# Performance work log

Measured on AMD Instinct MI355X. Metric: run time of the kernel, lower is better.

The kernel has to match this reference:

```python
import jax, jax.numpy as jnp
import numpy as np

D_MODEL = 1024
D_HIDDEN = 2048
BATCH = 2
SEQ = 4096


def setup_inputs() -> dict:
    key = jax.random.key(0)
    ks = jax.random.split(key, 14)
    d, h = D_MODEL, D_HIDDEN
    s_d = 1.0 / np.sqrt(d)
    s_h = 1.0 / np.sqrt(h)
    x = jax.random.normal(ks[0], (BATCH, SEQ, d), jnp.float32)
    W1 = jax.random.normal(ks[1], (d, d), jnp.float32) * s_d
    W2 = jax.random.normal(ks[2], (d, d), jnp.float32) * s_d
    Wlast = jax.random.normal(ks[3], (d, d), jnp.float32) * s_d
    conv_w = jax.random.normal(ks[4], (d, 1, 3), jnp.float32) * 0.5  # depthwise (O, I/g=1, K)
    conv_b = jnp.zeros((d,), jnp.float32)
    A = jax.random.normal(ks[5], (h,), jnp.float32)
    Wb = jax.random.normal(ks[6], (h, d), jnp.float32) * s_d
    bb = jnp.zeros((h,), jnp.float32)
    Wc = jax.random.normal(ks[7], (d, h), jnp.float32) * s_h
    bc = jnp.zeros((d,), jnp.float32)
    Wd = jax.random.normal(ks[8], (d, d), jnp.float32) * s_d
    bd = jnp.zeros((d,), jnp.float32)
    # small delta so cumsum(delta*A) over SEQ steps stays O(1) (avoids exp overflow)
    Wdelta = jax.random.normal(ks[9], (h, d), jnp.float32) * 0.01
    bdelta = jnp.full((h,), -8.0, jnp.float32)
    return dict(x=x, W1=W1, conv_w=conv_w, conv_b=conv_b, A=A, Wb=Wb, bb=bb,
                Wc=Wc, bc=bc, Wd=Wd, bd=bd, Wdelta=Wdelta, bdelta=bdelta,
                W2=W2, Wlast=Wlast)


def reference(x, W1, conv_w, conv_b, A, Wb, bb, Wc, bc, Wd, bd, Wdelta, bdelta, W2, Wlast):
    # x: [B, L, d]
    x1 = x @ W1.T  # linear1 (no bias)
    # depthwise conv1d, kernel 3, pad 1, groups = d_model
    xc = jax.lax.conv_general_dilated(
        x1.transpose(0, 2, 1), conv_w,
        window_strides=(1,), padding=[(1, 1)],
        feature_group_count=D_MODEL,
        dimension_numbers=('NCH', 'OIH', 'NCH')) + conv_b[None, :, None]
    xa = jax.nn.silu(xc.transpose(0, 2, 1))  # [B, L, d]
    # SSM: delta/A/B discretization + cumprod-cumsum scan along sequence
    delta = jax.nn.softplus(xa @ Wdelta.T + bdelta)  # [B, L, h]
    A_bar = jnp.exp(delta * A)
    B_bar = delta * (xa @ Wb.T + bb)
    A_cum = jnp.cumprod(A_bar, axis=1)
    h_st = jnp.cumsum(B_bar / A_cum, axis=1) * A_cum  # [B, L, h]
    out_ssm = (h_st @ Wc.T + bc) + (xa @ Wd.T + bd)  # [B, L, d]
    # gated residual
    x_res = jax.nn.silu(out_ssm @ W2.T)
    z = out_ssm * x_res
    return out_ssm + z @ Wlast.T
```

## Files before the change

kernel.cpp:

```cpp
#include <hip/hip_runtime.h>
#include <cstdint>
#include <cstddef>

#define DMODEL 1024
#define DH 2048
#define BATCH 2
#define SEQ 4096
#define MROWS (BATCH*SEQ)
#define CHUNK 64
#define NCHUNK (SEQ/CHUNK)

typedef unsigned short u16;
typedef unsigned int u32;
typedef __attribute__((ext_vector_type(8))) short bf16x8;
typedef __attribute__((ext_vector_type(4))) float f32x4;

__device__ __forceinline__ u16 f2bf(float f) {
    union { float f; unsigned u; } v; v.f = f;
    unsigned r = v.u + 0x7FFFu + ((v.u >> 16) & 1u);
    return (u16)(r >> 16);
}
__device__ __forceinline__ float bf2f(u16 h) {
    union { unsigned u; float f; } v; v.u = ((unsigned)h) << 16; return v.f;
}

__device__ __forceinline__ float softplus_fast(float x) {
    if (x < -4.f) return __expf(x);
    return (x > 0.f) ? (x + log1pf(__expf(-x))) : log1pf(__expf(x));
}
__device__ __forceinline__ float silu_fast(float v) {
    return v * __fdividef(1.f, 1.f + __expf(-v));
}

__global__ void cvt_bf16(const float* __restrict__ src, u16* __restrict__ dst, int n4) {
    int i = blockIdx.x * blockDim.x + threadIdx.x;
    if (i >= n4) return;
    const float4 v = reinterpret_cast<const float4*>(src)[i];
    ushort4 o;
    o.x = f2bf(v.x); o.y = f2bf(v.y); o.z = f2bf(v.z); o.w = f2bf(v.w);
    reinterpret_cast<ushort4*>(dst)[i] = o;
}

struct CvtArgs {
    const float* src[7];
    u16* dst[7];
    unsigned cum[8];
};
__global__ void cvt_multi(CvtArgs a) {
    const unsigned i = blockIdx.x * blockDim.x + threadIdx.x;
    if (i >= a.cum[7]) return;
    int s = 0;
    while (i >= a.cum[s+1]) ++s;
    const unsigned off = i - a.cum[s];
    const float4 v = reinterpret_cast<const float4*>(a.src[s])[off];
    ushort4 o;
    o.x = f2bf(v.x); o.y = f2bf(v.y); o.z = f2bf(v.z); o.w = f2bf(v.w);
    reinterpret_cast<ushort4*>(a.dst[s])[off] = o;
}

__device__ __forceinline__ void gload_lds16(const void* g, void* l) {
    __builtin_amdgcn_global_load_lds(
        (const __attribute__((address_space(1))) void*)g,
        (__attribute__((address_space(3))) void*)l,
        16, 0, 0);
}

template<int EP, bool TWOK, int BN>
__global__ __launch_bounds__(256, 4) void gemm_bt(
    const u16* __restrict__ A1, const u16* __restrict__ B1, int K1,
    const u16* __restrict__ A2, const u16* __restrict__ B2, int K2,
    float* __restrict__ C, u16* __restrict__ Cb, u16* __restrict__ Cb2,
    const float* __restrict__ bias, const float* __restrict__ bias2,
    const u16* __restrict__ aux,
    int M, int N)
{
    constexpr int FN   = BN / 32;
    constexpr int EPS  = BN + 4;
    constexpr int SMEM = (BN == 128) ? 40960 : 24576;
    __shared__ __align__(16) char smem[SMEM];
    u16* As = (u16*)smem;
    u16* Bs = (u16*)(smem + 16384);
    float* ep = (float*)smem;

    const int tid = threadIdx.x;

    const int nwg = gridDim.x * gridDim.y;
    int wg = blockIdx.y * gridDim.x + blockIdx.x;
    wg = (wg & 7) * (nwg >> 3) + (wg >> 3);
    const int stile = wg >> 6;
    const int t64   = wg & 63;
    const int nSn   = gridDim.x >> 3;
    const int sm = (nSn > 0) ? stile / nSn : stile;
    const int sn = (nSn > 0) ? stile - sm * nSn : 0;
    const int m0 = (sm * 8 + (t64 >> 3)) * 128;
    const int n0 = (sn * 8 + (t64 & 7)) * BN;

    const int wave = tid >> 6, lane = tid & 63;
    const int wr = (wave >> 1) * 64;
    const int wc = (wave & 1) * (BN / 2);
    const int fr = lane & 15, fq = lane >> 4;

    f32x4 acc[4][FN];
    #pragma unroll
    for (int m = 0; m < 4; m++)
        #pragma unroll
        for (int n = 0; n < FN; n++) acc[m][n] = f32x4{0.f, 0.f, 0.f, 0.f};

    auto run_seg = [&](const u16* __restrict__ A, const u16* __restrict__ B, int K) {
        const int nt = K >> 6;
        for (int t = 0; t < nt; ++t) {
            const int k0 = t << 6;
            #pragma unroll
            for (int i = 0; i < 4; ++i) {
                const int g = i*256 + tid;
                const int r = g >> 3;
                const int ch = (g & 7) ^ (r & 7);
                gload_lds16(A + (size_t)(m0 + r)*K + (k0 + ch*8), (char*)As + (size_t)g*16);
            }
            #pragma unroll
            for (int i = 0; i < BN/32; ++i) {
                const int g = i*256 + tid;
                const int r = g >> 3;
                const int ch = (g & 7) ^ (r & 7);
                gload_lds16(B + (size_t)(n0 + r)*K + (k0 + ch*8), (char*)Bs + (size_t)g*16);
            }
            __syncthreads();

            #pragma unroll
            for (int kk = 0; kk < 2; ++kk) {
                bf16x8 af[4], bfr[FN];
                #pragma unroll
                for (int m = 0; m < 4; m++) {
                    const int r = wr + m*16 + fr;
                    af[m] = *reinterpret_cast<const bf16x8*>(
                        (const char*)As + r*128 + (((kk*4 + fq) ^ (r & 7)) * 16));
                }
                #pragma unroll
                for (int n = 0; n < FN; n++) {
                    const int r = wc + n*16 + fr;
                    bfr[n] = *reinterpret_cast<const bf16x8*>(
                        (const char*)Bs + r*128 + (((kk*4 + fq) ^ (r & 7)) * 16));
                }
                #pragma unroll
                for (int m = 0; m < 4; m++)
                    #pragma unroll
                    for (int n = 0; n < FN; n++)
                        acc[m][n] = __builtin_amdgcn_mfma_f32_16x16x32_bf16(af[m], bfr[n], acc[m][n], 0, 0, 0);
            }
            __syncthreads();
        }
    };
    run_seg(A1, B1, K1);
    if constexpr (TWOK) run_seg(A2, B2, K2);

    const bool isDelta = (EP == 4) ? (n0 < DH) : false;
    #pragma unroll
    for (int c = 0; c < 2; ++c) {
        if ((wave >> 1) == c) {
            #pragma unroll
            for (int m = 0; m < 4; m++)
                #pragma unroll
                for (int n = 0; n < FN; n++) {
                    const int col = wc + n*16 + fr;
                    #pragma unroll
                    for (int j = 0; j < 4; j++)
                        ep[(m*16 + fq*4 + j)*EPS + col] = acc[m][n][j];
                }
        }
        __syncthreads();
        #pragma unroll
        for (int p = 0; p < BN/16; ++p) {
            const int idx = p*256 + tid;
            const int row = idx / (BN/4), c4 = idx % (BN/4);
            float4 v = *reinterpret_cast<const float4*>(&ep[row*EPS + c4*4]);
            const int rg   = m0 + c*64 + row;
            const int colg = n0 + c4*4;
            if constexpr (EP == 4) {
                const int cc = isDelta ? colg : (colg - DH);
                const float4 bv = *reinterpret_cast<const float4*>(
                    (isDelta ? bias : bias2) + cc);
                ushort4 o;
                if (isDelta) {
                    o.x = f2bf(softplus_fast(v.x + bv.x));
                    o.y = f2bf(softplus_fast(v.y + bv.y));
                    o.z = f2bf(softplus_fast(v.z + bv.z));
                    o.w = f2bf(softplus_fast(v.w + bv.w));
                } else {
                    o.x = f2bf(v.x + bv.x); o.y = f2bf(v.y + bv.y);
                    o.z = f2bf(v.z + bv.z); o.w = f2bf(v.w + bv.w);
                }
                *reinterpret_cast<ushort4*>((isDelta ? Cb : Cb2) + (size_t)rg*DH + cc) = o;
            } else {
                if (bias) {
                    const float4 b1 = *reinterpret_cast<const float4*>(bias + colg);
                    v.x += b1.x; v.y += b1.y; v.z += b1.z; v.w += b1.w;
                }
                if (bias2) {
                    const float4 b2 = *reinterpret_cast<const float4*>(bias2 + colg);
                    v.x += b2.x; v.y += b2.y; v.z += b2.z; v.w += b2.w;
                }
                const size_t gidx = (size_t)rg * N + colg;
                if constexpr (EP == 0) {
                    ushort4 o = { f2bf(v.x), f2bf(v.y), f2bf(v.z), f2bf(v.w) };
                    *reinterpret_cast<ushort4*>(Cb + gidx) = o;
                } else if constexpr (EP == 2) {
                    const ushort4 ab = *reinterpret_cast<const ushort4*>(aux + gidx);
                    ushort4 o = { f2bf(bf2f(ab.x) * silu_fast(v.x)),
                                  f2bf(bf2f(ab.y) * silu_fast(v.y)),
                                  f2bf(bf2f(ab.z) * silu_fast(v.z)),
                                  f2bf(bf2f(ab.w) * silu_fast(v.w)) };
                    *reinterpret_cast<ushort4*>(Cb + gidx) = o;
                } else {
                    const ushort4 ab = *reinterpret_cast<const ushort4*>(aux + gidx);
                    float4 o = { bf2f(ab.x) + v.x, bf2f(ab.y) + v.y,
                                 bf2f(ab.z) + v.z, bf2f(ab.w) + v.w };
                    *reinterpret_cast<float4*>(C + gidx) = o;
                }
            }
        }
        __syncthreads();
    }
}

__global__ void conv_silu8(const u16* __restrict__ x1, const float* __restrict__ cw,
                           const float* __restrict__ cb, u16* __restrict__ xab) {
    int t = blockIdx.x * blockDim.x + threadIdx.x;
    int c8  = t & (DMODEL/8 - 1);
    int row = t >> 7;
    int l = row & (SEQ - 1);
    const int c0 = c8 * 8;
    const size_t i0 = (size_t)row * DMODEL + c0;
    bf16x8 v0 = *reinterpret_cast<const bf16x8*>(x1 + i0);
    bf16x8 vm = {}; if (l > 0)       vm = *reinterpret_cast<const bf16x8*>(x1 + i0 - DMODEL);
    bf16x8 vp = {}; if (l < SEQ - 1) vp = *reinterpret_cast<const bf16x8*>(x1 + i0 + DMODEL);
    if (l == 0)       vm = bf16x8{};
    if (l == SEQ - 1) vp = bf16x8{};
    bf16x8 o;
    #pragma unroll
    for (int j = 0; j < 8; ++j) {
        const int c = c0 + j;
        float v = cw[c*3+0]*bf2f((u16)vm[j]) + cw[c*3+1]*bf2f((u16)v0[j])
                + cw[c*3+2]*bf2f((u16)vp[j]) + cb[c];
        o[j] = (short)f2bf(silu_fast(v));
    }
    *reinterpret_cast<bf16x8*>(xab + i0) = o;
}

__global__ void scan_chunks(const u16* __restrict__ delta, const u16* __restrict__ pBv,
                            const float* __restrict__ Avec,
                            float* __restrict__ cA, float* __restrict__ cB) {
    const int c = (blockIdx.x * blockDim.x + threadIdx.x) * 2;
    const int q = blockIdx.y;
    const int b = blockIdx.z;
    const float A0 = Avec[c], A1 = Avec[c+1];
    float hA0 = 1.f, hB0 = 0.f, hA1 = 1.f, hB1 = 0.f;
    size_t base = ((size_t)b*SEQ + q*CHUNK)*DH + c;
    for (int j = 0; j < CHUNK; ++j) {
        const u32 du = *reinterpret_cast<const u32*>(delta + base);
        const u32 pu = *reinterpret_cast<const u32*>(pBv + base);
        const float d0 = bf2f((u16)(du & 0xFFFF)), d1 = bf2f((u16)(du >> 16));
        const float p0 = bf2f((u16)(pu & 0xFFFF)), p1 = bf2f((u16)(pu >> 16));
        const float a0 = __expf(d0 * A0), a1 = __expf(d1 * A1);
        hA0 *= a0; hB0 = a0*hB0 + d0*p0;
        hA1 *= a1; hB1 = a1*hB1 + d1*p1;
        base += DH;
    }
    size_t o = ((size_t)b*NCHUNK + q)*DH + c;
    cA[o] = hA0; cA[o+1] = hA1;
    cB[o] = hB0; cB[o+1] = hB1;
}

__global__ void scan_prefix(const float* __restrict__ cA, const float* __restrict__ cB,
                            float* __restrict__ cH) {
    const int t = blockIdx.x * blockDim.x + threadIdx.x;
    const int b = t >> 11;
    const int c = t & (DH - 1);
    float h = 0.f;
    size_t o = ((size_t)b*NCHUNK)*DH + c;
    float a = cA[o], bb = cB[o];
    for (int q = 0; q < NCHUNK; ++q) {
        const size_t on = o + DH;
        float a2 = 0.f, b2 = 0.f;
        if (q + 1 < NCHUNK) { a2 = cA[on]; b2 = cB[on]; }
        cH[o] = h;
        h = a*h + bb;
        a = a2; bb = b2; o = on;
    }
}

__global__ void scan_apply(const u16* __restrict__ delta, const u16* __restrict__ pBv,
                           const float* __restrict__ Avec, const float* __restrict__ cH,
                           u16* __restrict__ hstb) {
    const int c = (blockIdx.x * blockDim.x + threadIdx.x) * 2;
    const int q = blockIdx.y;
    const int b = blockIdx.z;
    const float A0 = Avec[c], A1 = Avec[c+1];
    const size_t oh = ((size_t)b*NCHUNK + q)*DH + c;
    float h0 = cH[oh], h1 = cH[oh+1];
    size_t base = ((size_t)b*SEQ + q*CHUNK)*DH + c;
    for (int j = 0; j < CHUNK; ++j) {
        const u32 du = *reinterpret_cast<const u32*>(delta + base);
        const u32 pu = *reinterpret_cast<const u32*>(pBv + base);
        const float d0 = bf2f((u16)(du & 0xFFFF)), d1 = bf2f((u16)(du >> 16));
        const float p0 = bf2f((u16)(pu & 0xFFFF)), p1 = bf2f((u16)(pu >> 16));
        const float a0 = __expf(d0 * A0), a1 = __expf(d1 * A1);
        h0 = a0*h0 + d0*p0;
        h1 = a1*h1 + d1*p1;
        const u32 hv = (u32)f2bf(h0) | ((u32)f2bf(h1) << 16);
        *reinterpret_cast<u32*>(hstb + base) = hv;
        base += DH;
    }
}

extern "C" void kernel_launch(void* const* d_in, const int* in_sizes, int n_in,
                              void* d_out, int out_size, void* d_ws, size_t ws_size,
                              hipStream_t stream) {
    const float* x      = (const float*)d_in[0];
    const float* W1     = (const float*)d_in[1];
    const float* conv_w = (const float*)d_in[2];
    const float* conv_b = (const float*)d_in[3];
    const float* Avec   = (const float*)d_in[4];
    const float* Wb     = (const float*)d_in[5];
    const float* bb     = (const float*)d_in[6];
    const float* Wc     = (const float*)d_in[7];
    const float* bc     = (const float*)d_in[8];
    const float* Wd     = (const float*)d_in[9];
    const float* bd     = (const float*)d_in[10];
    const float* Wdelta = (const float*)d_in[11];
    const float* bdelta = (const float*)d_in[12];
    const float* W2     = (const float*)d_in[13];
    const float* Wlast  = (const float*)d_in[14];
    float* out = (float*)d_out;
    (void)in_sizes; (void)n_in; (void)out_size;

    struct Ptrs {
        u16 *w1, *wdel, *wb, *wd, *wc, *w2, *wl;
        float *cA, *cB, *cH;
        u16 *xb, *x1b, *xab, *delta, *pBv, *ossb, *hstb, *zb;
        size_t total;
    };
    auto layout = [&](int passes) -> Ptrs {
        Ptrs P{};
        const size_t Mp = MROWS / passes;
        const int nb = BATCH / passes;
        size_t off = 0;
        auto al = [&](size_t bytes) -> char* {
            char* p = (char*)d_ws + off; off += (bytes + 255) & ~(size_t)255; return p;
        };
        P.w1   = (u16*)al((size_t)DMODEL*DMODEL*2);
        P.wdel = (u16*)al((size_t)DH*DMODEL*2);
        P.wb   = (u16*)al((size_t)DH*DMODEL*2);
        P.wd   = (u16*)al((size_t)DMODEL*DMODEL*2);
        P.wc   = (u16*)al((size_t)DMODEL*DH*2);
        P.w2   = (u16*)al((size_t)DMODEL*DMODEL*2);
        P.wl   = (u16*)al((size_t)DMODEL*DMODEL*2);
        P.cA  = (float*)al((size_t)nb*NCHUNK*DH*4);
        P.cB  = (float*)al((size_t)nb*NCHUNK*DH*4);
        P.cH  = (float*)al((size_t)nb*NCHUNK*DH*4);
        char* RA = al(Mp*DMODEL*2);
        char* RB = al(Mp*DMODEL*2);
        char* RC = al(Mp*DMODEL*2);
        char* RD = al(Mp*DH*2);
        char* RE = al(Mp*DH*2);
        char* RF = al(Mp*DH*2);
        P.xb    = (u16*)RA; P.ossb = (u16*)RA;
        P.x1b   = (u16*)RB; P.zb   = (u16*)RB;
        P.xab   = (u16*)RC;
        P.delta = (u16*)RD;
        P.pBv   = (u16*)RE;
        P.hstb  = (u16*)RF;
        P.total = off;
        return P;
    };

    int passes = (ws_size >= layout(1).total) ? 1 : 2;
    Ptrs P = layout(passes);
    if (ws_size < P.total) return;
    const int Mp = MROWS / passes;
    const int nb = BATCH / passes;

    const dim3 blk(256);

    {
        CvtArgs a{};
        const float* srcs[7] = { W1, Wdelta, Wb, Wd, Wc, W2, Wlast };
        u16* dsts[7] = { P.w1, P.wdel, P.wb, P.wd, P.wc, P.w2, P.wl };
        const unsigned n4s[7] = {
            DMODEL*DMODEL/4, DH*DMODEL/4, DH*DMODEL/4, DMODEL*DMODEL/4,
            DMODEL*DH/4, DMODEL*DMODEL/4, DMODEL*DMODEL/4 };
        unsigned cum = 0;
        for (int s = 0; s < 7; ++s) { a.src[s] = srcs[s]; a.dst[s] = dsts[s]; a.cum[s] = cum; cum += n4s[s]; }
        a.cum[7] = cum;
        cvt_multi<<<dim3((cum + 255)/256), blk, 0, stream>>>(a);
    }

    const dim3 gS (DMODEL/64,  Mp/128);
    const dim3 gDB(2*DH/128,   Mp/128);

    for (int p = 0; p < passes; ++p) {
        const float* x_p  = x  + (size_t)p*Mp*DMODEL;
        float*      out_p = out + (size_t)p*Mp*DMODEL;

        {
            int n4 = (int)((size_t)Mp*DMODEL / 4);
            cvt_bf16<<<dim3((n4 + 255)/256), blk, 0, stream>>>(x_p, P.xb, n4);
        }
        gemm_bt<0,false,64><<<gS, blk, 0, stream>>>(P.xb, P.w1, DMODEL, nullptr, nullptr, 0,
                                                 nullptr, P.x1b, nullptr, nullptr, nullptr, nullptr, Mp, DMODEL);
        conv_silu8<<<dim3(Mp*DMODEL/8/256), blk, 0, stream>>>(P.x1b, conv_w, conv_b, P.xab);
        gemm_bt<4,false,128><<<gDB, blk, 0, stream>>>(P.xab, P.wdel, DMODEL, nullptr, nullptr, 0,
                                                  nullptr, P.delta, P.pBv, bdelta, bb, nullptr, Mp, 2*DH);
        scan_chunks<<<dim3(DH/2/256, NCHUNK, nb), blk, 0, stream>>>(P.delta, P.pBv, Avec, P.cA, P.cB);
        scan_prefix<<<dim3(nb*DH/256), blk, 0, stream>>>(P.cA, P.cB, P.cH);
        scan_apply <<<dim3(DH/2/256, NCHUNK, nb), blk, 0, stream>>>(P.delta, P.pBv, Avec, P.cH, P.hstb);
        gemm_bt<0,true,64><<<gS, blk, 0, stream>>>(P.xab, P.wd, DMODEL, P.hstb, P.wc, DH,
                                                nullptr, P.ossb, nullptr, bd, bc, nullptr, Mp, DMODEL);
        gemm_bt<2,false,64><<<gS, blk, 0, stream>>>(P.ossb, P.w2, DMODEL, nullptr, nullptr, 0,
                                                 nullptr, P.zb, nullptr, nullptr, nullptr, P.ossb, Mp, DMODEL);
        gemm_bt<3,false,64><<<gS, blk, 0, stream>>>(P.zb, P.wl, DMODEL, nullptr, nullptr, 0,
                                                 out_p, nullptr, nullptr, nullptr, nullptr, P.ossb, Mp, DMODEL);
    }
}
```

Baseline: 298.5 us.

## Double-buffer GEMM K-loop with BK=32 to overlap loads and MFMA

Result: slower. 338.3 us (+13.4%).

```diff
diff --git a/kernel.cpp b/kernel.cpp
--- a/kernel.cpp
+++ b/kernel.cpp
@@ -76,10 +76,9 @@
 {
     constexpr int FN   = BN / 32;
     constexpr int EPS  = BN + 4;
+    constexpr int BSZ  = BN * 64;
     constexpr int SMEM = (BN == 128) ? 40960 : 24576;
     __shared__ __align__(16) char smem[SMEM];
-    u16* As = (u16*)smem;
-    u16* Bs = (u16*)(smem + 16384);
     float* ep = (float*)smem;
 
     const int tid = threadIdx.x;
@@ -107,51 +106,66 @@
         for (int n = 0; n < FN; n++) acc[m][n] = f32x4{0.f, 0.f, 0.f, 0.f};
 
     auto run_seg = [&](const u16* __restrict__ A, const u16* __restrict__ B, int K) {
-        const int nt = K >> 6;
+        const int nt = K >> 5;
+        auto stage = [&](int t, int buf) {
+            const int k0 = t << 5;
+            #pragma unroll
+            for (int i = 0; i < 2; ++i) {
+                const int g = i*256 + tid;
+                const int r = g >> 2;
+                const int ch = (g & 3) ^ (r & 3);
+                gload_lds16(A + (size_t)(m0 + r)*K + (k0 + ch*8),
+                            smem + buf*8192 + (size_t)g*16);
+            }
+            #pragma unroll
+            for (int i = 0; i < BN/64; ++i) {
+                const int g = i*256 + tid;
+                const int r = g >> 2;
+                const int ch = (g & 3) ^ (r & 3);
+                gload_lds16(B + (size_t)(n0 + r)*K + (k0 + ch*8),
+                            smem + 16384 + buf*BSZ + (size_t)g*16);
+            }
+        };
+        auto compute = [&](int buf) {
+            const char* Ab = smem + buf*8192;
+            const char* Bb = smem + 16384 + buf*BSZ;
+            bf16x8 af[4], bfr[FN];
+            #pragma unroll
+            for (int m = 0; m < 4; m++) {
+                const int r = wr + m*16 + fr;
+                af[m] = *reinterpret_cast<const bf16x8*>(
+                    Ab + r*64 + (((fq) ^ (r & 3)) * 16));
+            }
+            #pragma unroll
+            for (int n = 0; n < FN; n++) {
+                const int r = wc + n*16 + fr;
+                bfr[n] = *reinterpret_cast<const bf16x8*>(
+                    Bb + r*64 + (((fq) ^ (r & 3)) * 16));
+            }
+            #pragma unroll
+            for (int m = 0; m < 4; m++)
+                #pragma unroll
+                for (int n = 0; n < FN; n++)
+                    acc[m][n] = __builtin_amdgcn_mfma_f32_16x16x32_bf16(af[m], bfr[n], acc[m][n], 0, 0, 0);
+        };
+
+        stage(0, 0);
+        asm volatile("s_waitcnt vmcnt(0)" ::: "memory");
+        __builtin_amdgcn_s_barrier();
+        __builtin_amdgcn_sched_barrier(0);
+        int buf = 0;
         for (int t = 0; t < nt; ++t) {
-            const int k0 = t << 6;
-            #pragma unroll
-            for (int i = 0; i < 4; ++i) {
-                const int g = i*256 + tid;
-                const int r = g >> 3;
-                const int ch = (g & 7) ^ (r & 7);
-                gload_lds16(A + (size_t)(m0 + r)*K + (k0 + ch*8), (char*)As + (size_t)g*16);
-            }
-            #pragma unroll
-            for (int i = 0; i < BN/32; ++i) {
-                const int g = i*256 + tid;
-                const int r = g >> 3;
-                const int ch = (g & 7) ^ (r & 7);
-                gload_lds16(B + (size_t)(n0 + r)*K + (k0 + ch*8), (char*)Bs + (size_t)g*16);
-            }
-            __syncthreads();
-
-            #pragma unroll
-            for (int kk = 0; kk < 2; ++kk) {
-                bf16x8 af[4], bfr[FN];
-                #pragma unroll
-                for (int m = 0; m < 4; m++) {
-                    const int r = wr + m*16 + fr;
-                    af[m] = *reinterpret_cast<const bf16x8*>(
-                        (const char*)As + r*128 + (((kk*4 + fq) ^ (r & 7)) * 16));
-                }
-                #pragma unroll
-                for (int n = 0; n < FN; n++) {
-                    const int r = wc + n*16 + fr;
-                    bfr[n] = *reinterpret_cast<const bf16x8*>(
-                        (const char*)Bs + r*128 + (((kk*4 + fq) ^ (r & 7)) * 16));
-                }
-                #pragma unroll
-                for (int m = 0; m < 4; m++)
-                    #pragma unroll
-                    for (int n = 0; n < FN; n++)
-                        acc[m][n] = __builtin_amdgcn_mfma_f32_16x16x32_bf16(af[m], bfr[n], acc[m][n], 0, 0, 0);
-            }
-            __syncthreads();
+            if (t + 1 < nt) stage(t + 1, buf ^ 1);
+            compute(buf);
+            asm volatile("s_waitcnt vmcnt(0)" ::: "memory");
+            __builtin_amdgcn_s_barrier();
+            __builtin_amdgcn_sched_barrier(0);
+            buf ^= 1;
         }
     };
     run_seg(A1, B1, K1);
     if constexpr (TWOK) run_seg(A2, B2, K2);
+    __syncthreads();
 
     const bool isDelta = (EP == 4) ? (n0 < DH) : false;
     #pragma unroll
```
